# Kernel tuning notes

Measured on AMD Instinct MI355X. Metric: run time of the kernel, lower is better.

The kernel has to match this reference:

```python
import jax, jax.numpy as jnp
import numpy as np

T = 32768          # number of t_eval points, dt = 30 s
BATCH = 32         # batched initial conditions
N_ROOMS = 16
N_STATE = N_ROOMS + 2
HID = 16
T0 = 259200.0      # start time (seconds); kept small so fp32 resolves 30 s steps
DT_GRID = 30.0
MU, STD = 23.359, 1.41      # state normalization for policy input
Q_VALUE = -16914.0          # cooling power per unit action
DAY = 86400.0
WEEK = 604800.0
A_SCALE, A_DIAG, B_SCALE = 1e-4, 1e-3, 1e-6


def setup_inputs() -> dict:
    key = jax.random.key(0)
    ks = jax.random.split(key, 8)
    t_eval = (T0 + DT_GRID * jnp.arange(T)).astype(jnp.float32)
    iv = 26.0 + jax.random.normal(ks[0], (BATCH, N_STATE), jnp.float32)
    W_A = jax.random.normal(ks[1], (N_STATE, N_STATE), jnp.float32)
    W_B = jax.random.normal(ks[2], (N_STATE, 1 + N_ROOMS), jnp.float32)
    W1 = jax.random.normal(ks[3], (HID, N_STATE + 2), jnp.float32)
    b1 = jax.random.normal(ks[4], (HID,), jnp.float32)
    w2 = jax.random.normal(ks[5], (HID,), jnp.float32)
    b2 = jax.random.normal(ks[6], (1,), jnp.float32)
    # outside-temperature table on a 30 s grid covering t_eval plus the +600 s tail
    Tout_table = 10.0 + 10.0 * jax.random.uniform(ks[7], (T + 21,), jnp.float32)
    return dict(t_eval=t_eval, iv=iv, W_A=W_A, W_B=W_B, W1=W1, b1=b1,
                w2=w2, b2=b2, Tout_table=Tout_table)


def reference(t_eval, iv, W_A, W_B, W1, b1, w2, b2, Tout_table):
    n = iv.shape[-1]
    A = A_SCALE * W_A - A_DIAG * jnp.eye(n, dtype=W_A.dtype)   # stable dynamics
    Bm = B_SCALE * W_B                                         # [n, 1+n_rooms]
    b_tout = Bm[:, 0]                                          # Tout column of B
    b_rooms = Q_VALUE * jnp.sum(Bm[:, 1:], axis=1)             # B @ (Q*ones) per unit action
    t0 = t_eval[0]
    nT = Tout_table.shape[0]

    def tout(t):  # linear interp of outside temperature at absolute time t
        pos = (t - t0) / DT_GRID
        i = jnp.clip(jnp.floor(pos).astype(jnp.int32), 0, nT - 2)
        fr = pos - i.astype(pos.dtype)
        return (1.0 - fr) * Tout_table[i] + fr * Tout_table[i + 1]

    def policy(t, x):  # deterministic cooling action in (0,1), per batch element
        tod = jnp.mod(t, DAY) / DAY
        tow = jnp.mod(t + 3.0 * DAY, WEEK) / WEEK   # epoch day 0 is a Thursday
        feats = jnp.broadcast_to(jnp.stack([tow, tod]).astype(x.dtype), (x.shape[0], 2))
        s = jnp.concatenate([(x - MU) / STD, feats], axis=1)   # [B, n+2]
        h = jnp.tanh(s @ W1.T + b1)
        return jax.nn.sigmoid(h @ w2 + b2[0])                  # [B]

    def f(t, x, act):  # dx/dt = A x + B u,  u = [Tout, Q*ones(n_rooms)]
        Bu = tout(t) * b_tout[None, :] + act[:, None] * b_rooms[None, :]
        return x @ A.T + Bu

    def step(x, ts):  # one fixed-step RK4 step; action held over the step (>=30 s gate)
        t, tn = ts
        dt = tn - t
        act = policy(t, x)
        k1 = f(t, x, act)
        k2 = f(t + 0.5 * dt, x + 0.5 * dt * k1, act)
        k3 = f(t + 0.5 * dt, x + 0.5 * dt * k2, act)
        k4 = f(tn, x + dt * k3, act)
        xn = x + (dt / 6.0) * (k1 + 2.0 * k2 + 2.0 * k3 + k4)
        return xn, xn

    _, xs = jax.lax.scan(step, iv, (t_eval[:-1], t_eval[1:]))
    return jnp.concatenate([iv[None], xs], axis=0)   # [T, batch, n_state]
```

## Files before the change

### kernel.cpp

```cpp
#include <hip/hip_runtime.h>

#define NSTATE 18
#define NBATCH 32
#define TSTEPS 32768
#define SEGS   64
#define SEGLEN 512
#define BURN   192

typedef float v2f __attribute__((ext_vector_type(2)));

#define PKFMA(ACC, Gp, Xp) \
  asm("v_pk_fma_f32 %0, %1, %2, %0" : "+v"(ACC) : "v"(Gp), "v"(Xp))

template <int CTRL>
__device__ __forceinline__ float dpp_xadd(float x) {
  int y = __builtin_amdgcn_update_dpp(0, __float_as_int(x), CTRL, 0xF, 0xF, true);
  return x + __int_as_float(y);
}

#define STEP(XI, XO, M, DOSTORE)                                                  \
  do {                                                                            \
    float tb0v = ldsT[(M)];                                                       \
    float tb1v = ldsT[(M) + 1];                                                   \
    v2f acc0, acc1;                                                               \
    acc0.x = fmaf(tb0v, d0, bb);                                                  \
    acc0.y = tb1v * d1;                                                           \
    acc1.x = (float)uw * e0c;                                                     \
    acc1.y = (float)ut * e1c;                                                     \
    PKFMA(acc0, G2[0], XI[0]); PKFMA(acc1, G2[1], XI[1]);                         \
    PKFMA(acc0, G2[2], XI[2]); PKFMA(acc1, G2[3], XI[3]);                         \
    PKFMA(acc0, G2[4], XI[4]); PKFMA(acc1, G2[5], XI[5]);                         \
    PKFMA(acc0, G2[6], XI[6]); PKFMA(acc1, G2[7], XI[7]);                         \
    PKFMA(acc0, G2[8], XI[8]);                                                    \
    v2f accs = acc0 + acc1;                                                       \
    float r = accs.x + accs.y;                                                    \
    float q2 = fmaf(aprev, ac2, r);         \
    xbuf[wIdx] = q2;         \
    XO[0] = *(const v2f*)(xbuf + 0);  XO[1] = *(const v2f*)(xbuf + 2);            \
    XO[2] = *(const v2f*)(xbuf + 4);  XO[3] = *(const v2f*)(xbuf + 6);            \
    XO[4] = *(const v2f*)(xbuf + 8);  XO[5] = *(const v2f*)(xbuf + 10);           \
    XO[6] = *(const v2f*)(xbuf + 12); XO[7] = *(const v2f*)(xbuf + 14);           \
    XO[8] = *(const v2f*)(xbuf + 16);                                             \
    float e2 = exp2f(q2);                 \
    float rc = __builtin_amdgcn_rcpf(1.0f + e2);                                  \
    float p = fmaf(nw2, rc, w2l);                             \
    p = dpp_xadd<0xB1>(p);                                                        \
    p = dpp_xadd<0x4E>(p);                                                        \
    p = dpp_xadd<0x141>(p);                                                       \
    p = dpp_xadd<0x140>(p);                                                       \
    float ez = exp2f(fmaf(p, -1.44269504f, nb2));                                 \
    float an = __builtin_amdgcn_rcpf(1.0f + ez);                                  \
    float anew = __int_as_float(__builtin_amdgcn_readlane(__float_as_int(an), 32)); \
    if (DOSTORE) {                                                                \
      if (L < NSTATE) ob[L] = fmaf(anew, cact, q2);                               \
      ob += NBATCH * NSTATE;                               \
    }                                                                             \
    aprev = anew;                                                                 \
    ut += 30u; if (ut >= 86400u) ut -= 86400u;                                    \
    uw += 30u; if (uw >= 604800u) uw -= 604800u;                                  \
  } while (0)

__global__ __launch_bounds__(64) void rc_run(
    const float* __restrict__ WA, const float* __restrict__ WB,
    const float* __restrict__ W1, const float* __restrict__ b1,
    const float* __restrict__ w2, const float* __restrict__ b2,
    const float* __restrict__ iv, const float* __restrict__ tout,
    float* __restrict__ out) {
  __shared__ double DB[1296 + 54];
  double* A  = DB;
  double* A2 = DB + 324;
  double* A3 = DB + 648;
  double* A4 = DB + 972;
  double* bt = DB + 1296;
  double* br = DB + 1314;
  double* cvs = DB + 1332;
  __shared__ __align__(16) float xbuf[96];

  const int L = threadIdx.x;
  const int idx = blockIdx.x;
  const int b = idx & (NBATCH - 1);
  const int s = idx >> 5;
  const double dt = 30.0;
  const float PS = 2.88539008f;

  const int ks   = s * SEGLEN;
  const int kend = min(TSTEPS - 1, ks + SEGLEN);
  const int kb   = max(0, ks - BURN);
  const int mBurn = ks - kb;
  const int mEnd  = kend - kb;

  for (int t = L; t < 324; t += 64) {
    int i = t / 18, j = t % 18;
    A[t] = 1e-4 * (double)WA[t] - (i == j ? 1e-3 : 0.0);
  }
  if (L < NSTATE) {
    bt[L] = 1e-6 * (double)WB[L * 17 + 0];
    double ssum = 0.0;
    for (int c = 1; c < 17; ++c) ssum += (double)WB[L * 17 + c];
    br[L] = -16914.0 * 1e-6 * ssum;
  }
  __syncthreads();
  for (int t = L; t < 324; t += 64) {
    int i = t / 18, j = t % 18;
    double s2 = 0.0;
    for (int l = 0; l < 18; ++l) s2 += A[i * 18 + l] * A[l * 18 + j];
    A2[t] = s2;
  }
  __syncthreads();
  for (int t = L; t < 324; t += 64) {
    int i = t / 18, j = t % 18;
    double s3 = 0.0, s4 = 0.0;
    for (int l = 0; l < 18; ++l) {
      s3 += A2[i * 18 + l] * A[l * 18 + j];
      s4 += A2[i * 18 + l] * A2[l * 18 + j];
    }
    A3[t] = s3;
    A4[t] = s4;
  }
  __syncthreads();
  if (L < NSTATE) {
    double s2 = 0.0;
    for (int j = 0; j < 18; ++j) {
      double m = (dt / 6.0) * ((L == j ? 6.0 : 0.0) + 3.0 * dt * A[L * 18 + j] +
                               dt * dt * A2[L * 18 + j] +
                               0.25 * dt * dt * dt * A3[L * 18 + j]);
      s2 += m * br[j];
    }
    cvs[L] = s2;
  }
  __syncthreads();

  v2f G2[9];
  float d0 = 0.f, d1 = 0.f, cact = 0.f, bb = 0.f, e0c = 0.f, e1c = 0.f,
        w2l = 0.f, ac2 = 0.f;
  const float b2v = b2[0];
  if (L < NSTATE) {
    double pcv = 0.0, dd0 = 0.0, dd1 = 0.0;
    for (int j = 0; j < 18; ++j) {
      double phi = (L == j ? 1.0 : 0.0) + dt * A[L * 18 + j] +
                   (dt * dt / 2.0) * A2[L * 18 + j] +
                   (dt * dt * dt / 6.0) * A3[L * 18 + j] +
                   (dt * dt * dt * dt / 24.0) * A4[L * 18 + j];
      if (j & 1) G2[j >> 1].y = (float)phi; else G2[j >> 1].x = (float)phi;
      pcv += phi * cvs[j];
      double m1 = (dt / 6.0) * ((L == j ? 1.0 : 0.0) + dt * A[L * 18 + j] +
                                0.5 * dt * dt * A2[L * 18 + j] +
                                0.25 * dt * dt * dt * A3[L * 18 + j]);
      double m23 = (dt / 6.0) * ((L == j ? 4.0 : 0.0) + 2.0 * dt * A[L * 18 + j] +
                                 0.5 * dt * dt * A2[L * 18 + j]);
      double m4 = (L == j ? dt / 6.0 : 0.0);
      dd0 += (m1 + 0.5 * m23) * bt[j];
      dd1 += (0.5 * m23 + m4) * bt[j];
    }
    cact = (float)cvs[L];
    ac2 = (float)pcv;
    d0 = (float)dd0;
    d1 = (float)dd1;
  } else if (L >= 32 && L < 48) {
    int m = L - 32;
    double ssum = 0.0, wc = 0.0;
    for (int j = 0; j < 18; ++j) {
      double g = (double)W1[m * 20 + j] / 1.41 * (double)PS;
      if (j & 1) G2[j >> 1].y = (float)g; else G2[j >> 1].x = (float)g;
      ssum += (double)W1[m * 20 + j];
      wc += g * cvs[j];
    }
    bb = (float)(((double)b1[m] - ssum * (23.359 / 1.41)) * (double)PS);
    e0c = W1[m * 20 + 18] * PS * (1.0f / 604800.0f);
    e1c = W1[m * 20 + 19] * PS * (1.0f / 86400.0f);
    w2l = w2[m];
    ac2 = (float)wc;
  } else {
#pragma unroll
    for (int j = 0; j < 9; ++j) { G2[j].x = 0.f; G2[j].y = 0.f; }
  }
  const float nw2 = -2.0f * w2l;
  const float nb2 = -1.44269504f * b2v;
  __syncthreads();

  float* ldsT = (float*)DB;
  const int cnt = mEnd + 2;
  for (int i = L; i < cnt; i += 64) ldsT[i] = tout[kb + i];

  float q = (L < NSTATE) ? iv[b * NSTATE + L] : 0.0f;
  if (s == 0 && L < NSTATE) out[b * NSTATE + L] = q;

  float aprev = 0.0f;
  unsigned ut = (30u * (unsigned)kb) % 86400u;
  unsigned uw = (518400u + 30u * (unsigned)kb) % 604800u;

  float* ob = out + (size_t)(ks + 1) * (NBATCH * NSTATE) + b * NSTATE;

  const int wIdx = (L < NSTATE) ? L : (32 + L);
  xbuf[wIdx] = q;
  v2f X[9], Y[9];
  X[0] = *(const v2f*)(xbuf + 0);  X[1] = *(const v2f*)(xbuf + 2);
  X[2] = *(const v2f*)(xbuf + 4);  X[3] = *(const v2f*)(xbuf + 6);
  X[4] = *(const v2f*)(xbuf + 8);  X[5] = *(const v2f*)(xbuf + 10);
  X[6] = *(const v2f*)(xbuf + 12); X[7] = *(const v2f*)(xbuf + 14);
  X[8] = *(const v2f*)(xbuf + 16);

  int m = 0;
  for (; m + 1 < mBurn; m += 2) {
    STEP(X, Y, m, false);
    STEP(Y, X, m + 1, false);
  }
  for (; m + 1 < mEnd; m += 2) {
    STEP(X, Y, m, true);
    STEP(Y, X, m + 1, true);
  }
  if (m < mEnd) {
    STEP(X, Y, m, true);
  }
}

extern "C" void kernel_launch(void* const* d_in, const int* in_sizes, int n_in,
                              void* d_out, int out_size, void* d_ws, size_t ws_size,
                              hipStream_t stream) {
  const float* iv = (const float*)d_in[1];
  const float* WA = (const float*)d_in[2];
  const float* WB = (const float*)d_in[3];
  const float* W1 = (const float*)d_in[4];
  const float* b1 = (const float*)d_in[5];
  const float* w2 = (const float*)d_in[6];
  const float* b2 = (const float*)d_in[7];
  const float* tout = (const float*)d_in[8];
  float* out = (float*)d_out;

  rc_run<<<NBATCH * SEGS, 64, 0, stream>>>(WA, WB, W1, b1, w2, b2, iv, tout, out);
}
```

Before: 270.2 us.

## Advance two RK4 steps per iteration using squared propagator and dual policy lanes

Restructures the serial recurrence so each loop iteration advances the state by two time steps. It precomputes Phi^2 and the propagated forcing and action vectors in double precision, and evaluates the second step's policy in a separate lane group (48-63) using W1*Phi. The goal is to halve the number of LDS broadcast round-trips of the serial state vector. Each iteration now carries two chained policy evaluations, more setup math, a longer burn-in and a shifted last segment. This adds packed FMAs with op_sel and raises fp32 error from the longer propagation.

```diff
diff --git a/kernel.cpp b/kernel.cpp
--- a/kernel.cpp
+++ b/kernel.cpp
@@ -5,12 +5,16 @@
 #define TSTEPS 32768
 #define SEGS   64
 #define SEGLEN 512
-#define BURN   192
+#define BURN   256
 
 typedef float v2f __attribute__((ext_vector_type(2)));
 
-#define PKFMA(ACC, Gp, Xp) \
-  asm("v_pk_fma_f32 %0, %1, %2, %0" : "+v"(ACC) : "v"(Gp), "v"(Xp))
+#define PKFMA_LO(ACC, Gp, Xp) \
+  asm("v_pk_fma_f32 %0, %1, %2, %0 op_sel:[0,0,0] op_sel_hi:[1,0,1]" \
+      : "+v"(ACC) : "v"(Gp), "v"(Xp))
+#define PKFMA_HI(ACC, Gp, Xp) \
+  asm("v_pk_fma_f32 %0, %1, %2, %0 op_sel:[0,1,0] op_sel_hi:[1,1,1]" \
+      : "+v"(ACC) : "v"(Gp), "v"(Xp))
 
 template <int CTRL>
 __device__ __forceinline__ float dpp_xadd(float x) {
@@ -18,46 +22,65 @@
   return x + __int_as_float(y);
 }
 
-#define STEP(XI, XO, M, DOSTORE)                                                  \
+#define STEPP(XI, XO, P, DOSTORE)                                                 \
   do {                                                                            \
-    float tb0v = ldsT[(M)];                                                       \
-    float tb1v = ldsT[(M) + 1];                                                   \
-    v2f acc0, acc1;                                                               \
-    acc0.x = fmaf(tb0v, d0, bb);                                                  \
-    acc0.y = tb1v * d1;                                                           \
-    acc1.x = (float)uw * e0c;                                                     \
-    acc1.y = (float)ut * e1c;                                                     \
-    PKFMA(acc0, G2[0], XI[0]); PKFMA(acc1, G2[1], XI[1]);                         \
-    PKFMA(acc0, G2[2], XI[2]); PKFMA(acc1, G2[3], XI[3]);                         \
-    PKFMA(acc0, G2[4], XI[4]); PKFMA(acc1, G2[5], XI[5]);                         \
-    PKFMA(acc0, G2[6], XI[6]); PKFMA(acc1, G2[7], XI[7]);                         \
-    PKFMA(acc0, G2[8], XI[8]);                                                    \
-    v2f accs = acc0 + acc1;                                                       \
-    float r = accs.x + accs.y;                                                    \
-    float q2 = fmaf(aprev, ac2, r);         \
-    xbuf[wIdx] = q2;         \
+    v2f t01 = *(const v2f*)(ldsT + 2 * (P));                                      \
+    float t2v = ldsT[2 * (P) + 2];                                                \
+    float fw = (float)uw, ft = (float)ut;                                         \
+    float ilo = fmaf(t01.x, C0.x, fmaf(t01.y, C1.x, fmaf(t2v, C2lo, CBlo)));      \
+    ilo = fmaf(fw, CWlo, ilo);                                                    \
+    ilo = fmaf(ft, CTlo, ilo);                                                    \
+    ilo = fmaf(a0p, F0.x, ilo);                                                   \
+    ilo = fmaf(a1p, F1.x, ilo);                                                   \
+    float ihi = fmaf(t01.x, C0.y, t01.y * C1.y);                                  \
+    ihi = fmaf(a0p, F0.y, ihi);                                                   \
+    ihi = fmaf(a1p, F1.y, ihi);                                                   \
+    v2f accA; accA.x = ilo; accA.y = ihi;                                         \
+    v2f accB; accB.x = 0.0f; accB.y = 0.0f;                                       \
+    PKFMA_LO(accA, G[0],  XI[0]);  PKFMA_HI(accB, G[1],  XI[0]);                  \
+    PKFMA_LO(accA, G[2],  XI[1]);  PKFMA_HI(accB, G[3],  XI[1]);                  \
+    PKFMA_LO(accA, G[4],  XI[2]);  PKFMA_HI(accB, G[5],  XI[2]);                  \
+    PKFMA_LO(accA, G[6],  XI[3]);  PKFMA_HI(accB, G[7],  XI[3]);                  \
+    PKFMA_LO(accA, G[8],  XI[4]);  PKFMA_HI(accB, G[9],  XI[4]);                  \
+    PKFMA_LO(accA, G[10], XI[5]);  PKFMA_HI(accB, G[11], XI[5]);                  \
+    PKFMA_LO(accA, G[12], XI[6]);  PKFMA_HI(accB, G[13], XI[6]);                  \
+    PKFMA_LO(accA, G[14], XI[7]);  PKFMA_HI(accB, G[15], XI[7]);                  \
+    PKFMA_LO(accA, G[16], XI[8]);  PKFMA_HI(accB, G[17], XI[8]);                  \
+    v2f acc = accA + accB;                                                        \
+    float vlo = acc.x, vhi = acc.y;                                               \
+    xbuf[wIdx] = vlo;              \
     XO[0] = *(const v2f*)(xbuf + 0);  XO[1] = *(const v2f*)(xbuf + 2);            \
     XO[2] = *(const v2f*)(xbuf + 4);  XO[3] = *(const v2f*)(xbuf + 6);            \
     XO[4] = *(const v2f*)(xbuf + 8);  XO[5] = *(const v2f*)(xbuf + 10);           \
     XO[6] = *(const v2f*)(xbuf + 12); XO[7] = *(const v2f*)(xbuf + 14);           \
     XO[8] = *(const v2f*)(xbuf + 16);                                             \
-    float e2 = exp2f(q2);                 \
+    float e2 = exp2f(vlo);                                                        \
     float rc = __builtin_amdgcn_rcpf(1.0f + e2);                                  \
-    float p = fmaf(nw2, rc, w2l);                             \
-    p = dpp_xadd<0xB1>(p);                                                        \
-    p = dpp_xadd<0x4E>(p);                                                        \
-    p = dpp_xadd<0x141>(p);                                                       \
-    p = dpp_xadd<0x140>(p);                                                       \
-    float ez = exp2f(fmaf(p, -1.44269504f, nb2));                                 \
+    float pA = fmaf(nw2A, rc, w2A);                                               \
+    pA = dpp_xadd<0xB1>(pA); pA = dpp_xadd<0x4E>(pA);                             \
+    pA = dpp_xadd<0x141>(pA); pA = dpp_xadd<0x140>(pA);                           \
+    float ez = exp2f(fmaf(pA, -1.44269504f, nb2));                                \
     float an = __builtin_amdgcn_rcpf(1.0f + ez);                                  \
-    float anew = __int_as_float(__builtin_amdgcn_readlane(__float_as_int(an), 32)); \
+    float aj0 = __int_as_float(__builtin_amdgcn_readlane(__float_as_int(an), 32));\
+    float qB = fmaf(aj0, uB, vlo);                                                \
+    float e2b = exp2f(qB);                                                        \
+    float rcb = __builtin_amdgcn_rcpf(1.0f + e2b);                                \
+    float pB = fmaf(nw2B, rcb, w2B);                                              \
+    pB = dpp_xadd<0xB1>(pB); pB = dpp_xadd<0x4E>(pB);                             \
+    pB = dpp_xadd<0x141>(pB); pB = dpp_xadd<0x140>(pB);                           \
+    float ezb = exp2f(fmaf(pB, -1.44269504f, nb2));                               \
+    float anb = __builtin_amdgcn_rcpf(1.0f + ezb);                                \
+    float aj1 = __int_as_float(__builtin_amdgcn_readlane(__float_as_int(anb), 48));\
     if (DOSTORE) {                                                                \
-      if (L < NSTATE) ob[L] = fmaf(anew, cact, q2);                               \
-      ob += NBATCH * NSTATE;                               \
+      if (L < NSTATE) {                                                           \
+        ob[L] = fmaf(aj0, cact, vhi);                               \
+        ob[L + 576] = fmaf(aj1, cact, fmaf(aj0, pcact, vlo));       \
+      }                                                                           \
+      ob += 1152;                                                                 \
     }                                                                             \
-    aprev = anew;                                                                 \
-    ut += 30u; if (ut >= 86400u) ut -= 86400u;                                    \
-    uw += 30u; if (uw >= 604800u) uw -= 604800u;                                  \
+    a0p = aj0; a1p = aj1;                                                         \
+    ut += 60u; if (ut >= 86400u) ut -= 86400u;                                    \
+    uw += 60u; if (uw >= 604800u) uw -= 604800u;                                  \
   } while (0)
 
 __global__ __launch_bounds__(64) void rc_run(
@@ -66,14 +89,19 @@
     const float* __restrict__ w2, const float* __restrict__ b2,
     const float* __restrict__ iv, const float* __restrict__ tout,
     float* __restrict__ out) {
-  __shared__ double DB[1296 + 54];
-  double* A  = DB;
-  double* A2 = DB + 324;
-  double* A3 = DB + 648;
-  double* A4 = DB + 972;
-  double* bt = DB + 1296;
-  double* br = DB + 1314;
-  double* cvs = DB + 1332;
+  __shared__ double DB[1440];
+  double* A   = DB;
+  double* A2  = DB + 324;
+  double* A3  = DB + 648;
+  double* A4  = DB + 972;
+  double* bt  = DB + 1296;
+  double* br  = DB + 1314;
+  double* cv  = DB + 1332;
+  double* d0v = DB + 1350;
+  double* d1v = DB + 1368;
+  double* pc1 = DB + 1386;
+  double* pc2 = DB + 1404;
+  double* pc3 = DB + 1422;
   __shared__ __align__(16) float xbuf[96];
 
   const int L = threadIdx.x;
@@ -83,11 +111,10 @@
   const double dt = 30.0;
   const float PS = 2.88539008f;
 
-  const int ks   = s * SEGLEN;
-  const int kend = min(TSTEPS - 1, ks + SEGLEN);
-  const int kb   = max(0, ks - BURN);
+  const int ks = (s == 63) ? (TSTEPS - 1 - SEGLEN) : s * SEGLEN;
+  const int kb = max(0, ks - BURN);
   const int mBurn = ks - kb;
-  const int mEnd  = kend - kb;
+  const int mEnd = (ks + SEGLEN) - kb;
 
   for (int t = L; t < 324; t += 64) {
     int i = t / 18, j = t % 18;
@@ -119,30 +146,12 @@
   }
   __syncthreads();
   if (L < NSTATE) {
-    double s2 = 0.0;
+    double sc = 0.0, dd0 = 0.0, dd1 = 0.0;
     for (int j = 0; j < 18; ++j) {
       double m = (dt / 6.0) * ((L == j ? 6.0 : 0.0) + 3.0 * dt * A[L * 18 + j] +
                                dt * dt * A2[L * 18 + j] +
                                0.25 * dt * dt * dt * A3[L * 18 + j]);
-      s2 += m * br[j];
-    }
-    cvs[L] = s2;
-  }
-  __syncthreads();
-
-  v2f G2[9];
-  float d0 = 0.f, d1 = 0.f, cact = 0.f, bb = 0.f, e0c = 0.f, e1c = 0.f,
-        w2l = 0.f, ac2 = 0.f;
-  const float b2v = b2[0];
-  if (L < NSTATE) {
-    double pcv = 0.0, dd0 = 0.0, dd1 = 0.0;
-    for (int j = 0; j < 18; ++j) {
-      double phi = (L == j ? 1.0 : 0.0) + dt * A[L * 18 + j] +
-                   (dt * dt / 2.0) * A2[L * 18 + j] +
-                   (dt * dt * dt / 6.0) * A3[L * 18 + j] +
-                   (dt * dt * dt * dt / 24.0) * A4[L * 18 + j];
-      if (j & 1) G2[j >> 1].y = (float)phi; else G2[j >> 1].x = (float)phi;
-      pcv += phi * cvs[j];
+      sc += m * br[j];
       double m1 = (dt / 6.0) * ((L == j ? 1.0 : 0.0) + dt * A[L * 18 + j] +
                                 0.5 * dt * dt * A2[L * 18 + j] +
                                 0.25 * dt * dt * dt * A3[L * 18 + j]);
@@ -152,40 +161,105 @@
       dd0 += (m1 + 0.5 * m23) * bt[j];
       dd1 += (0.5 * m23 + m4) * bt[j];
     }
-    cact = (float)cvs[L];
-    ac2 = (float)pcv;
-    d0 = (float)dd0;
-    d1 = (float)dd1;
+    cv[L] = sc;
+    d0v[L] = dd0;
+    d1v[L] = dd1;
+  }
+  __syncthreads();
+  for (int t = L; t < 324; t += 64) {
+    int i = t / 18, j = t % 18;
+    A[t] = (i == j ? 1.0 : 0.0) + dt * A[t] + (dt * dt / 2.0) * A2[t] +
+           (dt * dt * dt / 6.0) * A3[t] + (dt * dt * dt * dt / 24.0) * A4[t];
+  }
+  __syncthreads();
+  for (int t = L; t < 324; t += 64) {
+    int i = t / 18, j = t % 18;
+    double s2 = 0.0;
+    for (int l = 0; l < 18; ++l) s2 += A[i * 18 + l] * A[l * 18 + j];
+    A2[t] = s2;
+  }
+  __syncthreads();
+  if (L < NSTATE) { double s1 = 0.0; for (int j = 0; j < 18; ++j) s1 += A[L * 18 + j] * cv[j];  pc1[L] = s1; }
+  __syncthreads();
+  if (L < NSTATE) { double s1 = 0.0; for (int j = 0; j < 18; ++j) s1 += A[L * 18 + j] * pc1[j]; pc2[L] = s1; }
+  __syncthreads();
+  if (L < NSTATE) { double s1 = 0.0; for (int j = 0; j < 18; ++j) s1 += A[L * 18 + j] * pc2[j]; pc3[L] = s1; }
+  __syncthreads();
+
+  v2f G[18];
+  v2f F0; F0.x = 0.f; F0.y = 0.f;
+  v2f F1; F1.x = 0.f; F1.y = 0.f;
+  v2f C0; C0.x = 0.f; C0.y = 0.f;
+  v2f C1; C1.x = 0.f; C1.y = 0.f;
+  float C2lo = 0.f, CWlo = 0.f, CTlo = 0.f, CBlo = 0.f;
+  float cact = 0.f, pcact = 0.f, uB = 0.f;
+  float w2A = 0.f, nw2A = 0.f, w2B = 0.f, nw2B = 0.f;
+  const float b2v = b2[0];
+  const float nb2 = -1.44269504f * b2v;
+
+  if (L < NSTATE) {
+    for (int j = 0; j < 18; ++j) { G[j].x = (float)A2[L * 18 + j]; G[j].y = (float)A[L * 18 + j]; }
+    double pd0 = 0.0, pd1 = 0.0;
+    for (int j = 0; j < 18; ++j) { pd0 += A[L * 18 + j] * d0v[j]; pd1 += A[L * 18 + j] * d1v[j]; }
+    C0.x = (float)pd0;            C0.y = (float)d0v[L];
+    C1.x = (float)(pd1 + d0v[L]); C1.y = (float)d1v[L];
+    C2lo = (float)d1v[L];
+    F0.x = (float)pc3[L]; F0.y = (float)pc2[L];
+    F1.x = (float)pc2[L]; F1.y = (float)pc1[L];
+    cact = (float)cv[L];
+    pcact = (float)pc1[L];
   } else if (L >= 32 && L < 48) {
     int m = L - 32;
-    double ssum = 0.0, wc = 0.0;
+    double f0 = 0.0, f1 = 0.0, ssum = 0.0;
     for (int j = 0; j < 18; ++j) {
-      double g = (double)W1[m * 20 + j] / 1.41 * (double)PS;
-      if (j & 1) G2[j >> 1].y = (float)g; else G2[j >> 1].x = (float)g;
+      double g = (double)W1[m * 20 + j] * ((double)PS / 1.41);
+      G[j].x = (float)g; G[j].y = 0.f;
+      f0 += g * pc1[j];
+      f1 += g * cv[j];
       ssum += (double)W1[m * 20 + j];
-      wc += g * cvs[j];
     }
-    bb = (float)(((double)b1[m] - ssum * (23.359 / 1.41)) * (double)PS);
-    e0c = W1[m * 20 + 18] * PS * (1.0f / 604800.0f);
-    e1c = W1[m * 20 + 19] * PS * (1.0f / 86400.0f);
-    w2l = w2[m];
-    ac2 = (float)wc;
+    F0.x = (float)f0; F1.x = (float)f1;
+    CBlo = (float)(((double)b1[m] - ssum * (23.359 / 1.41)) * (double)PS);
+    CWlo = W1[m * 20 + 18] * PS * (1.0f / 604800.0f);
+    CTlo = W1[m * 20 + 19] * PS * (1.0f / 86400.0f);
+    w2A = w2[m]; nw2A = -2.0f * w2A;
+  } else if (L >= 48) {
+    int m = L - 48;
+    double f0 = 0.0, f1 = 0.0, ub = 0.0, ssum = 0.0, wd0 = 0.0, wd1 = 0.0;
+    for (int j = 0; j < 18; ++j) {
+      double g = (double)W1[m * 20 + j] * ((double)PS / 1.41);
+      double wp = 0.0;
+      for (int k = 0; k < 18; ++k)
+        wp += (double)W1[m * 20 + k] * ((double)PS / 1.41) * A[k * 18 + j];
+      G[j].x = (float)wp; G[j].y = 0.f;
+      f0 += g * pc2[j];
+      f1 += g * pc1[j];
+      ub += g * cv[j];
+      wd0 += g * d0v[j];
+      wd1 += g * d1v[j];
+      ssum += (double)W1[m * 20 + j];
+    }
+    F0.x = (float)f0; F1.x = (float)f1; uB = (float)ub;
+    C0.x = (float)wd0; C1.x = (float)wd1;
+    CWlo = W1[m * 20 + 18] * PS * (1.0f / 604800.0f);
+    CTlo = W1[m * 20 + 19] * PS * (1.0f / 86400.0f);
+    CBlo = (float)(((double)b1[m] - ssum * (23.359 / 1.41)) * (double)PS) +
+           30.0f * CWlo + 30.0f * CTlo;
+    w2B = w2[m]; nw2B = -2.0f * w2B;
   } else {
-#pragma unroll
-    for (int j = 0; j < 9; ++j) { G2[j].x = 0.f; G2[j].y = 0.f; }
-  }
-  const float nw2 = -2.0f * w2l;
-  const float nb2 = -1.44269504f * b2v;
+    for (int j = 0; j < 18; ++j) { G[j].x = 0.f; G[j].y = 0.f; }
+  }
   __syncthreads();
 
   float* ldsT = (float*)DB;
   const int cnt = mEnd + 2;
   for (int i = L; i < cnt; i += 64) ldsT[i] = tout[kb + i];
+  __syncthreads();
 
   float q = (L < NSTATE) ? iv[b * NSTATE + L] : 0.0f;
   if (s == 0 && L < NSTATE) out[b * NSTATE + L] = q;
 
-  float aprev = 0.0f;
+  float a0p = 0.0f, a1p = 0.0f;
   unsigned ut = (30u * (unsigned)kb) % 86400u;
   unsigned uw = (518400u + 30u * (unsigned)kb) % 604800u;
 
@@ -200,17 +274,16 @@
   X[6] = *(const v2f*)(xbuf + 12); X[7] = *(const v2f*)(xbuf + 14);
   X[8] = *(const v2f*)(xbuf + 16);
 
-  int m = 0;
-  for (; m + 1 < mBurn; m += 2) {
-    STEP(X, Y, m, false);
-    STEP(Y, X, m + 1, false);
-  }
-  for (; m + 1 < mEnd; m += 2) {
-    STEP(X, Y, m, true);
-    STEP(Y, X, m + 1, true);
-  }
-  if (m < mEnd) {
-    STEP(X, Y, m, true);
+  const int nburn = mBurn >> 1;
+  const int ntot = mEnd >> 1;
+  int p = 0;
+  for (; p < nburn; p += 2) {
+    STEPP(X, Y, p, false);
+    STEPP(Y, X, p + 1, false);
+  }
+  for (; p < ntot; p += 2) {
+    STEPP(X, Y, p, true);
+    STEPP(Y, X, p + 1, true);
   }
 }
 
```

New measurement: 269.2 us. No clear change (-0.4%).
